# Performance work log

Measured on AMD Instinct MI355X. Metric: run time of the kernel, lower is better.

Reference implementation:

```python
import jax, jax.numpy as jnp
import numpy as np

B, V = 256, 128000

def setup_inputs() -> dict:
    key = jax.random.key(0)
    k1, k2, k3 = jax.random.split(key, 3)
    logits = jax.random.normal(k1, (B, V), dtype=jnp.float32)
    temperatures = jax.random.uniform(k2, (B,), dtype=jnp.float32)
    top_ps = jax.random.uniform(k3, (B,), dtype=jnp.float32)
    return {"logits": logits, "temperatures": temperatures, "top_ps": top_ps}

def reference(logits, temperatures, top_ps):
    logits = logits.astype(jnp.float32)
    greedy_tokens = jnp.argmax(logits, axis=-1)
    t = temperatures[:, None]
    greedy_mask = t <= 1e-10                       # [B, 1]
    safe_t = jnp.maximum(t, 1e-5)
    probs = jax.nn.softmax(logits / safe_t, axis=-1)  # [B, V]
    # descending sort of probs with indices
    order = jnp.argsort(-probs, axis=-1)           # [B, V]
    sorted_probs = jnp.take_along_axis(probs, order, axis=-1)
    cum = jnp.cumsum(sorted_probs, axis=-1)
    mask = cum > top_ps[:, None]
    mask = mask.at[:, 0].set(False)                # always keep top-1
    sorted_probs = jnp.where(mask, 0.0, sorted_probs)
    # scatter the masked probs back to original vocab positions
    rows = jnp.arange(B)[:, None]
    probs = jnp.zeros_like(probs).at[rows, order].set(sorted_probs)
    probs = probs / jnp.sum(probs, axis=-1, keepdims=True)
    # Gumbel-max style sampling: argmax(probs / Exp(1) noise)
    noise = jax.random.exponential(jax.random.key(1), probs.shape, dtype=jnp.float32)
    noise = jnp.maximum(noise, 1e-10)
    sample_tokens = jnp.argmax(probs / noise, axis=-1)
    return jnp.where(greedy_mask[:, 0], greedy_tokens, sample_tokens)
```

## Files before the change

kernel.cpp:

```cpp
#include <hip/hip_runtime.h>
#include <stdint.h>

typedef unsigned long long u64;
typedef uint32_t u32;

#define BB 256
#define VV 128000
#define NV4 (VV / 4)
#define SLICES 16
#define SL4 (NV4 / SLICES)
#define NBUCK 4096
#define CAP 2048
#define QSCALE 1.099511627776e12f
#define QINV   (1.0 / 1099511627776.0)

#define OFF_SMAX 0
#define OFF_SARG (16*1024)
#define OFF_WWIN (32*1024)
#define OFF_PAR  (64*1024)
#define OFF_CNT  (72*1024)
#define OFF_HIST (80*1024)
#define OFF_LIST (OFF_HIST + (size_t)BB*NBUCK*8)
#define WS_TOTAL (OFF_LIST + (size_t)BB*CAP*8)

struct RowPar { int bstar; float thr; double M; double cutZ; };

#if defined(__has_builtin)
# if __has_builtin(__builtin_amdgcn_sched_barrier)
#  define SCHED_FENCE() __builtin_amdgcn_sched_barrier(0)
# endif
#endif
#ifndef SCHED_FENCE
# define SCHED_FENCE() asm volatile("" ::: "memory")
#endif

__device__ __forceinline__ u32 rotl32(u32 v, u32 r) { return (v << r) | (v >> (32u - r)); }

__device__ __forceinline__ u32 threefry_bits(u32 j) {
    const u32 ks0 = 0u, ks1 = 1u, ks2 = 0x1BD11BDBu;
    u32 x0 = ks0, x1 = j + ks1;
    x0 += x1; x1 = rotl32(x1, 13); x1 ^= x0;
    x0 += x1; x1 = rotl32(x1, 15); x1 ^= x0;
    x0 += x1; x1 = rotl32(x1, 26); x1 ^= x0;
    x0 += x1; x1 = rotl32(x1, 6);  x1 ^= x0;
    x0 += ks1; x1 += ks2 + 1u;
    x0 += x1; x1 = rotl32(x1, 17); x1 ^= x0;
    x0 += x1; x1 = rotl32(x1, 29); x1 ^= x0;
    x0 += x1; x1 = rotl32(x1, 16); x1 ^= x0;
    x0 += x1; x1 = rotl32(x1, 24); x1 ^= x0;
    x0 += ks2; x1 += ks0 + 2u;
    x0 += x1; x1 = rotl32(x1, 13); x1 ^= x0;
    x0 += x1; x1 = rotl32(x1, 15); x1 ^= x0;
    x0 += x1; x1 = rotl32(x1, 26); x1 ^= x0;
    x0 += x1; x1 = rotl32(x1, 6);  x1 ^= x0;
    x0 += ks0; x1 += ks1 + 3u;
    x0 += x1; x1 = rotl32(x1, 17); x1 ^= x0;
    x0 += x1; x1 = rotl32(x1, 29); x1 ^= x0;
    x0 += x1; x1 = rotl32(x1, 16); x1 ^= x0;
    x0 += x1; x1 = rotl32(x1, 24); x1 ^= x0;
    x0 += ks1; x1 += ks2 + 4u;
    x0 += x1; x1 = rotl32(x1, 13); x1 ^= x0;
    x0 += x1; x1 = rotl32(x1, 15); x1 ^= x0;
    x0 += x1; x1 = rotl32(x1, 26); x1 ^= x0;
    x0 += x1; x1 = rotl32(x1, 6);  x1 ^= x0;
    x0 += ks2; x1 += ks0 + 5u;
    return x0 ^ x1;
}

__device__ __forceinline__ float q_of(float x, float invT, float xm) {
    return __expf(fmaf(x, invT, -xm));
}

__device__ __forceinline__ float noise_of(u32 j) {
    u32 bits = threefry_bits(j);
    float u = __uint_as_float((bits >> 9) | 0x3F800000u) - 1.0f;
    return fmaxf(-log1pf(-u), 1e-10f);
}

extern "C" __global__ void __launch_bounds__(256, 1)
k1_stats(const float* __restrict__ logits, float* __restrict__ smax,
         int* __restrict__ sarg, u64* __restrict__ Whist, int* __restrict__ Wcnt) {
    int blk = blockIdx.x, r = blk >> 4, s = blk & 15;
    int tid = threadIdx.x, lane = tid & 63, wid = tid >> 6;
    __shared__ float sf[4]; __shared__ int si[4];
    Whist[(size_t)r * NBUCK + s * 256 + tid] = 0ULL;
    if (s == 0 && tid == 0) Wcnt[r] = 0;
    const float4* L4 = (const float4*)(logits + (size_t)r * VV);
    int i0 = s * SL4 + tid;
    bool h7 = tid < (SL4 - 7 * 256);
    float4 b0 = L4[i0],          b1 = L4[i0 + 256],  b2 = L4[i0 + 512];
    float4 b3 = L4[i0 + 768],    b4 = L4[i0 + 1024], b5 = L4[i0 + 1280];
    float4 b6 = L4[i0 + 1536],   b7 = L4[h7 ? i0 + 1792 : i0];
    SCHED_FENCE();
    float m = -3.402823466e38f; int mi = 0x7FFFFFFF;
    auto upd = [&](float4 a, int iv) {
        float m4 = fmaxf(fmaxf(a.x, a.y), fmaxf(a.z, a.w));
        if (m4 > m) {
            int base = iv * 4;
            if      (a.x == m4) mi = base;
            else if (a.y == m4) mi = base + 1;
            else if (a.z == m4) mi = base + 2;
            else                mi = base + 3;
            m = m4;
        }
    };
    upd(b0, i0);        upd(b1, i0 + 256);  upd(b2, i0 + 512);  upd(b3, i0 + 768);
    upd(b4, i0 + 1024); upd(b5, i0 + 1280); upd(b6, i0 + 1536);
    if (h7) upd(b7, i0 + 1792);
    for (int off = 32; off; off >>= 1) {
        float ov = __shfl_down(m, off); int oi = __shfl_down(mi, off);
        if (ov > m || (ov == m && oi < mi)) { m = ov; mi = oi; }
    }
    if (lane == 0) { sf[wid] = m; si[wid] = mi; }
    __syncthreads();
    if (tid == 0) {
        for (int w = 1; w < 4; w++) {
            float ov = sf[w]; int oi = si[w];
            if (ov > m || (ov == m && oi < mi)) { m = ov; mi = oi; }
        }
        smax[blk] = m; sarg[blk] = mi;
    }
}

extern "C" __global__ void __launch_bounds__(256, 1)
k2_hist(const float* __restrict__ logits, const float* __restrict__ smax,
        const float* __restrict__ temps, u64* __restrict__ Whist) {
    __shared__ u64 lh[NBUCK];
    int blk = blockIdx.x, r = blk >> 4, s = blk & 15, tid = threadIdx.x;
    for (int i = tid; i < NBUCK; i += 256) lh[i] = 0ULL;
    float T = fmaxf(temps[r], 1e-5f), invT = 1.0f / T;
    float rm = -3.402823466e38f;
    for (int j = 0; j < 16; j++) rm = fmaxf(rm, smax[r * 16 + j]);
    float xm = rm * invT;
    __syncthreads();
    const float4* L4 = (const float4*)(logits + (size_t)r * VV);
    int i0 = s * SL4 + tid;
    bool h7 = tid < (SL4 - 7 * 256);
    float4 b0 = L4[i0],          b1 = L4[i0 + 256],  b2 = L4[i0 + 512];
    float4 b3 = L4[i0 + 768],    b4 = L4[i0 + 1024], b5 = L4[i0 + 1280];
    float4 b6 = L4[i0 + 1536],   b7 = L4[h7 ? i0 + 1792 : i0];
    SCHED_FENCE();
    auto proc = [&](float4 x) {
        float xs[4] = {x.x, x.y, x.z, x.w};
        #pragma unroll
        for (int k = 0; k < 4; k++) {
            float t = fmaf(xs[k], invT, -xm);
            if (t < -104.0f) continue;
            float q = __expf(t);
            u32 pb = __float_as_uint(q);
            if (pb) atomicAdd(&lh[pb >> 18], (u64)(q * QSCALE));
        }
    };
    proc(b0); proc(b1); proc(b2); proc(b3); proc(b4); proc(b5); proc(b6);
    if (h7) proc(b7);
    __syncthreads();
    u64* gh = Whist + (size_t)r * NBUCK;
    for (int i = tid; i < NBUCK; i += 256) {
        u64 v = lh[i];
        if (v) atomicAdd(&gh[i], v);
    }
}

extern "C" __global__ void __launch_bounds__(1024)
k3_cut(const u64* __restrict__ Whist, const float* __restrict__ topps,
       RowPar* __restrict__ par) {
    int r = blockIdx.x, tid = threadIdx.x, lane = tid & 63, wid = tid >> 6;
    __shared__ double wtot[16];
    __shared__ double sh_cutZ; __shared__ int sh_b; __shared__ double sh_M;
    const u64* gh = Whist + (size_t)r * NBUCK;
    double h0 = (double)gh[4 * tid]     * QINV;
    double h1 = (double)gh[4 * tid + 1] * QINV;
    double h2 = (double)gh[4 * tid + 2] * QINV;
    double h3 = (double)gh[4 * tid + 3] * QINV;
    double s3 = h3, s2 = s3 + h2, s1 = s2 + h1, s0 = s1 + h0;
    double incl = s0;
    for (int off = 1; off < 64; off <<= 1) {
        double u = __shfl_down(incl, off);
        if (lane + off < 64) incl += u;
    }
    double excl = __shfl_down(incl, 1); if (lane == 63) excl = 0.0;
    if (lane == 0) wtot[wid] = incl;
    if (tid == 0) { sh_b = -1; sh_M = 0.0; }
    __syncthreads();
    double cw = 0.0;
    for (int w = wid + 1; w < 16; w++) cw += wtot[w];
    double carry = excl + cw;
    if (tid == 0) sh_cutZ = (double)topps[r] * (s0 + carry);
    __syncthreads();
    double cutZ = sh_cutZ;
    double S0 = s0 + carry, S1 = s1 + carry, S2 = s2 + carry, S3 = s3 + carry;
    if (S0 > cutZ && S1 <= cutZ)    { sh_b = 4 * tid;     sh_M = S1; }
    if (S1 > cutZ && S2 <= cutZ)    { sh_b = 4 * tid + 1; sh_M = S2; }
    if (S2 > cutZ && S3 <= cutZ)    { sh_b = 4 * tid + 2; sh_M = S3; }
    if (S3 > cutZ && carry <= cutZ) { sh_b = 4 * tid + 3; sh_M = carry; }
    __syncthreads();
    if (tid == 0) {
        float thr = -3.402823466e38f;
        if (sh_b > 0) {
            float qlo = __uint_as_float((u32)sh_b << 18);
            if (qlo >= 1.17549435e-38f) thr = logf(qlo) - 1e-3f;
        }
        RowPar p; p.bstar = sh_b; p.thr = thr; p.M = sh_M; p.cutZ = cutZ;
        par[r] = p;
    }
}

extern "C" __global__ void __launch_bounds__(256, 1)
k4_race(const float* __restrict__ logits, const float* __restrict__ smax,
        const float* __restrict__ temps, const RowPar* __restrict__ par,
        int* __restrict__ Wcnt, u64* __restrict__ Wlist, u64* __restrict__ Wwin) {
    int blk = blockIdx.x, r = blk >> 4, s = blk & 15;
    int tid = threadIdx.x, lane = tid & 63, wid = tid >> 6;
    __shared__ u64 seg[4][256];
    __shared__ u64 wred[4];
    float T = fmaxf(temps[r], 1e-5f), invT = 1.0f / T;
    float rm = -3.402823466e38f;
    for (int j = 0; j < 16; j++) rm = fmaxf(rm, smax[r * 16 + j]);
    float xm = rm * invT;
    int bstar = par[r].bstar;
    float thr = par[r].thr;
    const float4* L4 = (const float4*)(logits + (size_t)r * VV);
    u32 jbase = (u32)r * (u32)VV;
    u64 pk = 0ULL;
    const u64 lanelt = (1ULL << lane) - 1ULL;
    int i0 = s * SL4 + tid;
    bool h7 = tid < (SL4 - 7 * 256);
    float4 b0 = L4[i0],          b1 = L4[i0 + 256],  b2 = L4[i0 + 512];
    float4 b3 = L4[i0 + 768],    b4 = L4[i0 + 1024], b5 = L4[i0 + 1280];
    float4 b6 = L4[i0 + 1536],   b7 = L4[h7 ? i0 + 1792 : i0];
    SCHED_FENCE();

    auto chunk = [&](float4 v, int iv, bool valid) {
        float t0 = fmaf(v.x, invT, -xm), t1 = fmaf(v.y, invT, -xm);
        float t2 = fmaf(v.z, invT, -xm), t3 = fmaf(v.w, invT, -xm);
        float ts[4] = {t0, t1, t2, t3};
        int base = iv * 4;
        int wcount = 0;
        #pragma unroll
        for (int k = 0; k < 4; k++) {
            bool pass = valid && (ts[k] >= thr);
            u64 bm = __ballot(pass);
            if (pass) {
                int off = __popcll(bm & lanelt);
                seg[wid][wcount + off] =
                    ((u64)__float_as_uint(ts[k]) << 32) | (u32)(base + k);
            }
            wcount += __popcll(bm);
        }
        asm volatile("s_waitcnt lgkmcnt(0)" ::: "memory");
        for (int di = lane; di < wcount; di += 64) {
            u64 e = seg[wid][di];
            float tt = __uint_as_float((u32)(e >> 32));
            u32 dv = (u32)e;
            float q = __expf(tt);
            u32 pb = __float_as_uint(q);
            if (pb) {
                int b = (int)(pb >> 18);
                if (b > bstar) {
                    float nz = noise_of(jbase + dv);
                    float sc = __fdividef(q, nz);
                    u64 ee = ((u64)__float_as_uint(sc) << 32) | (u64)(~dv);
                    if (ee > pk) pk = ee;
                } else if (b == bstar) {
                    int pos = atomicAdd(&Wcnt[r], 1);
                    if (pos < CAP)
                        Wlist[(size_t)r * CAP + pos] = ((u64)pb << 32) | (u64)(~dv);
                }
            }
        }
    };
    chunk(b0, i0, true);        chunk(b1, i0 + 256, true);
    chunk(b2, i0 + 512, true);  chunk(b3, i0 + 768, true);
    chunk(b4, i0 + 1024, true); chunk(b5, i0 + 1280, true);
    chunk(b6, i0 + 1536, true); chunk(b7, i0 + 1792, h7);

    for (int off = 32; off; off >>= 1) { u64 o = __shfl_down(pk, off); if (o > pk) pk = o; }
    if (lane == 0) wred[wid] = pk;
    __syncthreads();
    if (tid == 0) {
        for (int w = 1; w < 4; w++) if (wred[w] > pk) pk = wred[w];
        Wwin[blk] = pk;
    }
}

extern "C" __global__ void __launch_bounds__(1024)
k5_final(const float* __restrict__ smax, const int* __restrict__ sarg,
         const float* __restrict__ temps, const float* __restrict__ topps,
         const RowPar* __restrict__ par, const int* __restrict__ Wcnt,
         const u64* __restrict__ Wlist, const u64* __restrict__ Wwin,
         int* __restrict__ out) {
    int r = blockIdx.x, tid = threadIdx.x, lane = tid & 63, wid = tid >> 6;
    __shared__ u64 sb[CAP];
    __shared__ double wtot[16];
    __shared__ u64 wred[16];
    __shared__ int sh_js, sh_n, sh_gidx; __shared__ float sh_rm;
    RowPar p = par[r];
    if (tid == 0) {
        float rm = -3.402823466e38f; int gi = 0x7FFFFFFF;
        for (int j = 0; j < 16; j++) {
            float v = smax[r * 16 + j];
            if (v > rm) { rm = v; gi = sarg[r * 16 + j]; }
        }
        sh_rm = rm; sh_gidx = gi;
        int n = Wcnt[r]; if (n > CAP) n = CAP; sh_n = n;
        sh_js = 0x7FFFFFFF;
    }
    __syncthreads();
    int n = sh_n;
    int npad = 4; while (npad < n) npad <<= 1;
    const u64* lst = Wlist + (size_t)r * CAP;
    for (int i = tid; i < npad; i += 1024) sb[i] = (i < n) ? lst[i] : 0ULL;
    __syncthreads();
    for (int k = 2; k <= npad; k <<= 1) {
        for (int j = k >> 1; j > 0; j >>= 1) {
            for (int i = tid; i < npad; i += 1024) {
                int q2 = i ^ j;
                if (q2 > i) {
                    u64 a = sb[i], b = sb[q2];
                    bool desc = ((i & k) == 0);
                    if (desc ? (a < b) : (a > b)) { sb[i] = b; sb[q2] = a; }
                }
            }
            __syncthreads();
        }
    }
    int t2 = tid * 2;
    double f0 = 0.0, f1 = 0.0;
    if (t2 < npad) {
        f0 = (double)__uint_as_float((u32)(sb[t2] >> 32));
        f1 = (double)__uint_as_float((u32)(sb[t2 + 1] >> 32));
    }
    double c0 = f0, c1 = c0 + f1;
    double incl = c1;
    for (int off = 1; off < 64; off <<= 1) {
        double u = __shfl_up(incl, off);
        if (lane >= off) incl += u;
    }
    double excl = __shfl_up(incl, 1); if (lane == 0) excl = 0.0;
    double wt = __shfl(incl, 63);
    if (lane == 0) wtot[wid] = wt;
    __syncthreads();
    double cw = 0.0;
    for (int w = 0; w < wid; w++) cw += wtot[w];
    double cr = cw + excl;
    if (t2 < npad) {
        bool m0 = (p.M + (cr + c0)) > p.cutZ;
        bool m1 = (p.M + (cr + c1)) > p.cutZ;
        int cand = m0 ? t2 : m1 ? (t2 + 1) : 0x7FFFFFFF;
        if (cand != 0x7FFFFFFF) atomicMin(&sh_js, cand);
    }
    __syncthreads();
    float Traw = temps[r];
    if (tid == 0) {
        int js = sh_js; if (js > n) js = n;
        float T = fmaxf(Traw, 1e-5f), invT = 1.0f / T, xm = sh_rm * invT;
        int btop = (int)(__float_as_uint(q_of(sh_rm, invT, xm)) >> 18);
        if (js == 0 && p.bstar == btop) js = 1;
        sh_js = js;
    }
    __syncthreads();
    int js = sh_js;
    u32 jbase = (u32)r * (u32)VV;
    u64 pk = 0ULL;
    for (int i = tid; i < js; i += 1024) {
        u64 key = sb[i];
        float qq = __uint_as_float((u32)(key >> 32));
        u32 v = ~(u32)key;
        float nz = noise_of(jbase + v);
        float sc = __fdividef(qq, nz);
        u64 e = ((u64)__float_as_uint(sc) << 32) | (u64)(~v);
        if (e > pk) pk = e;
    }
    if (tid < 16) { u64 w = Wwin[r * 16 + tid]; if (w > pk) pk = w; }
    for (int off = 32; off; off >>= 1) { u64 o = __shfl_down(pk, off); if (o > pk) pk = o; }
    if (lane == 0) wred[wid] = pk;
    __syncthreads();
    if (tid == 0) {
        for (int w = 1; w < 16; w++) if (wred[w] > pk) pk = wred[w];
        int bi = (int)(~(u32)pk);
        out[r] = (Traw <= 1e-10f) ? sh_gidx : bi;
    }
}

extern "C" __global__ void __launch_bounds__(1024, 1)
sampler_fallback(const float* __restrict__ logits, const float* __restrict__ temps,
                 const float* __restrict__ topps, int* __restrict__ out)
{
    const int row = blockIdx.x;
    const int tid = threadIdx.x;
    const int lane = tid & 63;
    const int wid = tid >> 6;
    const float* L = logits + (size_t)row * VV;
    const float4* L4 = (const float4*)L;
    __shared__ __align__(16) unsigned char SMEM[32768];
    float* hist = (float*)SMEM;
    u64* sortbuf = (u64*)SMEM;
    __shared__ double wtot[16];
    __shared__ float wredf[16];
    __shared__ int wredi[16];
    __shared__ float sh_lmax;
    __shared__ int sh_gidx;
    __shared__ double sh_cutZ;
    __shared__ double sh_M;
    __shared__ int sh_bstar;
    __shared__ int sh_ng;
    __shared__ int sh_jstar;
    const float Traw = temps[row];
    const float T = fmaxf(Traw, 1e-5f);
    const float invT = 1.0f / T;
    const float tp = topps[row];
    float lmax = -3.402823466e38f; int lidx = 0x7FFFFFFF;
    for (int iv = tid; iv < NV4; iv += 1024) {
        float4 x = L4[iv];
        float m4 = fmaxf(fmaxf(x.x, x.y), fmaxf(x.z, x.w));
        if (m4 > lmax) {
            int base = iv * 4;
            if      (x.x == m4) lidx = base;
            else if (x.y == m4) lidx = base + 1;
            else if (x.z == m4) lidx = base + 2;
            else                lidx = base + 3;
            lmax = m4;
        }
    }
    for (int off = 32; off > 0; off >>= 1) {
        float ov = __shfl_down(lmax, off);
        int   oi = __shfl_down(lidx, off);
        if (ov > lmax || (ov == lmax && oi < lidx)) { lmax = ov; lidx = oi; }
    }
    if (lane == 0) { wredf[wid] = lmax; wredi[wid] = lidx; }
    for (int i = tid; i < NBUCK; i += 1024) hist[i] = 0.0f;
    __syncthreads();
    if (wid == 0) {
        float v = (lane < 16) ? wredf[lane] : -3.402823466e38f;
        int   i = (lane < 16) ? wredi[lane] : 0x7FFFFFFF;
        for (int off = 32; off > 0; off >>= 1) {
            float ov = __shfl_down(v, off);
            int   oi = __shfl_down(i, off);
            if (ov > v || (ov == v && oi < i)) { v = ov; i = oi; }
        }
        if (lane == 0) { sh_lmax = v; sh_gidx = i; }
    }
    __syncthreads();
    const float xm = sh_lmax * invT;
    const int gidx = sh_gidx;
    const int btop = (int)(__float_as_uint(q_of(sh_lmax, invT, xm)) >> 18);
    for (int iv = tid; iv < NV4; iv += 1024) {
        float4 x = L4[iv];
        float q0 = q_of(x.x, invT, xm), q1 = q_of(x.y, invT, xm);
        float q2 = q_of(x.z, invT, xm), q3 = q_of(x.w, invT, xm);
        u32 b0 = __float_as_uint(q0), b1 = __float_as_uint(q1);
        u32 b2 = __float_as_uint(q2), b3 = __float_as_uint(q3);
        if (b0) atomicAdd(&hist[b0 >> 18], q0);
        if (b1) atomicAdd(&hist[b1 >> 18], q1);
        if (b2) atomicAdd(&hist[b2 >> 18], q2);
        if (b3) atomicAdd(&hist[b3 >> 18], q3);
    }
    __syncthreads();
    float h0 = hist[4 * tid], h1 = hist[4 * tid + 1],
          h2 = hist[4 * tid + 2], h3 = hist[4 * tid + 3];
    double s3 = (double)h3, s2 = s3 + (double)h2, s1 = s2 + (double)h1, s0 = s1 + (double)h0;
    double incl = s0;
    for (int off = 1; off < 64; off <<= 1) {
        double u = __shfl_down(incl, off);
        if (lane + off < 64) incl += u;
    }
    double excl = __shfl_down(incl, 1);
    if (lane == 63) excl = 0.0;
    if (lane == 0) wtot[wid] = incl;
    __syncthreads();
    double cw = 0.0;
    for (int w = wid + 1; w < 16; w++) cw += wtot[w];
    const double carry = excl + cw;
    if (tid == 0) {
        sh_cutZ = (double)tp * (s0 + carry);
        sh_bstar = -1; sh_M = 0.0; sh_ng = 0; sh_jstar = 0x7FFFFFFF;
    }
    __syncthreads();
    const double cutZ = sh_cutZ;
    {
        double S0 = s0 + carry, S1 = s1 + carry, S2 = s2 + carry, S3 = s3 + carry;
        if (S0 > cutZ && S1 <= cutZ)    { sh_bstar = 4 * tid;     sh_M = S1; }
        if (S1 > cutZ && S2 <= cutZ)    { sh_bstar = 4 * tid + 1; sh_M = S2; }
        if (S2 > cutZ && S3 <= cutZ)    { sh_bstar = 4 * tid + 2; sh_M = S3; }
        if (S3 > cutZ && carry <= cutZ) { sh_bstar = 4 * tid + 3; sh_M = carry; }
    }
    __syncthreads();
    const int bstar = sh_bstar;
    const double M = sh_M;
    float bs = -1.0f; int bi = 0x7FFFFFFF;
    const u32 jbase = (u32)row * (u32)VV;
    for (int iv = tid; iv < NV4; iv += 1024) {
        float4 x = L4[iv];
        float qs[4] = {q_of(x.x, invT, xm), q_of(x.y, invT, xm),
                       q_of(x.z, invT, xm), q_of(x.w, invT, xm)};
        int base = iv * 4;
        #pragma unroll
        for (int k = 0; k < 4; k++) {
            u32 pb = __float_as_uint(qs[k]);
            if (pb == 0u) continue;
            int b = (int)(pb >> 18);
            if (b > bstar) {
                int v = base + k;
                float nz = noise_of(jbase + (u32)v);
                float sc = __fdividef(qs[k], nz);
                if (sc > bs || (sc == bs && v < bi)) { bs = sc; bi = v; }
            } else if (b == bstar) {
                int pos = atomicAdd(&sh_ng, 1);
                if (pos < 4096)
                    sortbuf[pos] = ((u64)pb << 32) | (u32)(~(u32)(base + k));
            }
        }
    }
    __syncthreads();
    if (bstar >= 0) {
        int n = sh_ng; if (n > 4096) n = 4096;
        int npad = 4; while (npad < n) npad <<= 1;
        for (int i = tid; i < npad; i += 1024) if (i >= n) sortbuf[i] = 0ULL;
        __syncthreads();
        for (int k = 2; k <= npad; k <<= 1) {
            for (int j = k >> 1; j > 0; j >>= 1) {
                for (int i = tid; i < npad; i += 1024) {
                    int pidx = i ^ j;
                    if (pidx > i) {
                        u64 a = sortbuf[i], b2 = sortbuf[pidx];
                        bool desc = ((i & k) == 0);
                        if (desc ? (a < b2) : (a > b2)) { sortbuf[i] = b2; sortbuf[pidx] = a; }
                    }
                }
                __syncthreads();
            }
        }
        double f0 = 0.0, f1 = 0.0, f2 = 0.0, f3 = 0.0;
        int t4 = tid * 4;
        if (t4 < npad) {
            f0 = (double)__uint_as_float((u32)(sortbuf[t4]     >> 32));
            f1 = (double)__uint_as_float((u32)(sortbuf[t4 + 1] >> 32));
            f2 = (double)__uint_as_float((u32)(sortbuf[t4 + 2] >> 32));
            f3 = (double)__uint_as_float((u32)(sortbuf[t4 + 3] >> 32));
        }
        double c0 = f0, c1 = c0 + f1, c2 = c1 + f2, c3 = c2 + f3;
        double incl2 = c3;
        for (int off = 1; off < 64; off <<= 1) {
            double u = __shfl_up(incl2, off);
            if (lane >= off) incl2 += u;
        }
        double excl2 = __shfl_up(incl2, 1);
        if (lane == 0) excl2 = 0.0;
        double wt = __shfl(incl2, 63);
        if (lane == 0) wtot[wid] = wt;
        __syncthreads();
        double cw2 = 0.0;
        for (int w = 0; w < wid; w++) cw2 += wtot[w];
        double cr = cw2 + excl2;
        if (t4 < npad) {
            bool m0 = (M + (cr + c0)) > cutZ;
            bool m1 = (M + (cr + c1)) > cutZ;
            bool m2 = (M + (cr + c2)) > cutZ;
            bool m3 = (M + (cr + c3)) > cutZ;
            int cand = m0 ? t4 : m1 ? (t4 + 1) : m2 ? (t4 + 2) : m3 ? (t4 + 3) : 0x7FFFFFFF;
            if (cand != 0x7FFFFFFF) atomicMin(&sh_jstar, cand);
        }
        __syncthreads();
        int jstar = sh_jstar; if (jstar > n) jstar = n;
        if (jstar == 0 && bstar == btop) jstar = 1;
        for (int i = tid; i < jstar; i += 1024) {
            u64 key = sortbuf[i];
            float qq = __uint_as_float((u32)(key >> 32));
            int v = (int)(~(u32)key);
            float nz = noise_of(jbase + (u32)v);
            float sc = __fdividef(qq, nz);
            if (sc > bs || (sc == bs && v < bi)) { bs = sc; bi = v; }
        }
    }
    for (int off = 32; off > 0; off >>= 1) {
        float ov = __shfl_down(bs, off);
        int   oi = __shfl_down(bi, off);
        if (ov > bs || (ov == bs && oi < bi)) { bs = ov; bi = oi; }
    }
    if (lane == 0) { wredf[wid] = bs; wredi[wid] = bi; }
    __syncthreads();
    if (tid == 0) {
        float v = wredf[0]; int i = wredi[0];
        for (int w = 1; w < 16; w++) {
            float ov = wredf[w]; int oi = wredi[w];
            if (ov > v || (ov == v && oi < i)) { v = ov; i = oi; }
        }
        out[row] = (Traw <= 1e-10f) ? gidx : i;
    }
}

extern "C" void kernel_launch(void* const* d_in, const int* in_sizes, int n_in,
                              void* d_out, int out_size, void* d_ws, size_t ws_size,
                              hipStream_t stream) {
    const float* logits = (const float*)d_in[0];
    const float* temps = (const float*)d_in[1];
    const float* topps = (const float*)d_in[2];
    int* out = (int*)d_out;
    (void)in_sizes; (void)n_in; (void)out_size;

    if (ws_size >= WS_TOTAL) {
        char* ws = (char*)d_ws;
        float* smax  = (float*)(ws + OFF_SMAX);
        int*   sarg  = (int*)(ws + OFF_SARG);
        u64*   wwin  = (u64*)(ws + OFF_WWIN);
        RowPar* par  = (RowPar*)(ws + OFF_PAR);
        int*   wcnt  = (int*)(ws + OFF_CNT);
        u64*   whist = (u64*)(ws + OFF_HIST);
        u64*   wlist = (u64*)(ws + OFF_LIST);
        k1_stats<<<BB * SLICES, 256, 0, stream>>>(logits, smax, sarg, whist, wcnt);
        k2_hist<<<BB * SLICES, 256, 0, stream>>>(logits, smax, temps, whist);
        k3_cut<<<BB, 1024, 0, stream>>>(whist, topps, par);
        k4_race<<<BB * SLICES, 256, 0, stream>>>(logits, smax, temps, par, wcnt, wlist, wwin);
        k5_final<<<BB, 1024, 0, stream>>>(smax, sarg, temps, topps, par, wcnt, wlist, wwin, out);
    } else {
        sampler_fallback<<<BB, 1024, 0, stream>>>(logits, temps, topps, out);
    }
}
```

Measured before the change: 368.9 us.

## Double-buffer survivor compaction across waves and tighten histogram exp cutoff

The race kernel now compacts threshold-passing logits into a double-buffered shared segment per wave. All 256 threads then process the survivors of all four waves together, with each thread taking up to four entries, while the next chunk is being filtered. This replaces per-wave serial loops that ran whole iterations for only a few survivors, and it balances the expensive noise and exp work across the block at the cost of a block-wide barrier per chunk. Separately, the histogram kernel skips elements with scaled logit below -27.75 instead of -104, so it does fewer exp and atomic operations. This drops tiny probabilities that may be below the quantization resolution, which could slightly change histogram mass.

```diff
diff --git a/kernel.cpp b/kernel.cpp
--- a/kernel.cpp
+++ b/kernel.cpp
@@ -145,7 +145,7 @@
         #pragma unroll
         for (int k = 0; k < 4; k++) {
             float t = fmaf(xs[k], invT, -xm);
-            if (t < -104.0f) continue;
+            if (t < -27.75f) continue;
             float q = __expf(t);
             u32 pb = __float_as_uint(q);
             if (pb) atomicAdd(&lh[pb >> 18], (u64)(q * QSCALE));
@@ -211,7 +211,8 @@
         int* __restrict__ Wcnt, u64* __restrict__ Wlist, u64* __restrict__ Wwin) {
     int blk = blockIdx.x, r = blk >> 4, s = blk & 15;
     int tid = threadIdx.x, lane = tid & 63, wid = tid >> 6;
-    __shared__ u64 seg[4][256];
+    __shared__ u64 seg[2][4][256];
+    __shared__ int qn[2][4];
     __shared__ u64 wred[4];
     float T = fmaxf(temps[r], 1e-5f), invT = 1.0f / T;
     float rm = -3.402823466e38f;
@@ -223,6 +224,7 @@
     u32 jbase = (u32)r * (u32)VV;
     u64 pk = 0ULL;
     const u64 lanelt = (1ULL << lane) - 1ULL;
+    const int dsg = tid & 3, idxb = tid >> 2;
     int i0 = s * SL4 + tid;
     bool h7 = tid < (SL4 - 7 * 256);
     float4 b0 = L4[i0],          b1 = L4[i0 + 256],  b2 = L4[i0 + 512];
@@ -230,49 +232,68 @@
     float4 b6 = L4[i0 + 1536],   b7 = L4[h7 ? i0 + 1792 : i0];
     SCHED_FENCE();
 
-    auto chunk = [&](float4 v, int iv, bool valid) {
+    auto kfilter = [&](int ph, float4 v, int off, bool valid) {
         float t0 = fmaf(v.x, invT, -xm), t1 = fmaf(v.y, invT, -xm);
         float t2 = fmaf(v.z, invT, -xm), t3 = fmaf(v.w, invT, -xm);
-        float ts[4] = {t0, t1, t2, t3};
-        int base = iv * 4;
-        int wcount = 0;
-        #pragma unroll
-        for (int k = 0; k < 4; k++) {
-            bool pass = valid && (ts[k] >= thr);
-            u64 bm = __ballot(pass);
-            if (pass) {
-                int off = __popcll(bm & lanelt);
-                seg[wid][wcount + off] =
-                    ((u64)__float_as_uint(ts[k]) << 32) | (u32)(base + k);
+        int base = (i0 + off) * 4;
+        bool p0 = valid && (t0 >= thr), p1 = valid && (t1 >= thr);
+        bool p2 = valid && (t2 >= thr), p3 = valid && (t3 >= thr);
+        u64 m0 = __ballot(p0), m1 = __ballot(p1);
+        u64 m2 = __ballot(p2), m3 = __ballot(p3);
+        int c0 = __popcll(m0), c01 = c0 + __popcll(m1), c012 = c01 + __popcll(m2);
+        u64* sg = seg[ph][wid];
+        if (p0) sg[       __popcll(m0 & lanelt)] = ((u64)__float_as_uint(t0) << 32) | (u32)(base + 0);
+        if (p1) sg[c0   + __popcll(m1 & lanelt)] = ((u64)__float_as_uint(t1) << 32) | (u32)(base + 1);
+        if (p2) sg[c01  + __popcll(m2 & lanelt)] = ((u64)__float_as_uint(t2) << 32) | (u32)(base + 2);
+        if (p3) sg[c012 + __popcll(m3 & lanelt)] = ((u64)__float_as_uint(t3) << 32) | (u32)(base + 3);
+        if (lane == 0) qn[ph][wid] = c012 + __popcll(m3);
+    };
+    auto kproc = [&](u64 e) {
+        float tt = __uint_as_float((u32)(e >> 32));
+        u32 dv = (u32)e;
+        float q = __expf(tt);
+        u32 pb = __float_as_uint(q);
+        if (pb) {
+            int b = (int)(pb >> 18);
+            if (b > bstar) {
+                float nz = noise_of(jbase + dv);
+                float sc = __fdividef(q, nz);
+                u64 ee = ((u64)__float_as_uint(sc) << 32) | (u64)(~dv);
+                if (ee > pk) pk = ee;
+            } else if (b == bstar) {
+                int pos = atomicAdd(&Wcnt[r], 1);
+                if (pos < CAP)
+                    Wlist[(size_t)r * CAP + pos] = ((u64)pb << 32) | (u64)(~dv);
             }
-            wcount += __popcll(bm);
-        }
-        asm volatile("s_waitcnt lgkmcnt(0)" ::: "memory");
-        for (int di = lane; di < wcount; di += 64) {
-            u64 e = seg[wid][di];
-            float tt = __uint_as_float((u32)(e >> 32));
-            u32 dv = (u32)e;
-            float q = __expf(tt);
-            u32 pb = __float_as_uint(q);
-            if (pb) {
-                int b = (int)(pb >> 18);
-                if (b > bstar) {
-                    float nz = noise_of(jbase + dv);
-                    float sc = __fdividef(q, nz);
-                    u64 ee = ((u64)__float_as_uint(sc) << 32) | (u64)(~dv);
-                    if (ee > pk) pk = ee;
-                } else if (b == bstar) {
-                    int pos = atomicAdd(&Wcnt[r], 1);
-                    if (pos < CAP)
-                        Wlist[(size_t)r * CAP + pos] = ((u64)pb << 32) | (u64)(~dv);
-                }
-            }
         }
     };
-    chunk(b0, i0, true);        chunk(b1, i0 + 256, true);
-    chunk(b2, i0 + 512, true);  chunk(b3, i0 + 768, true);
-    chunk(b4, i0 + 1024, true); chunk(b5, i0 + 1280, true);
-    chunk(b6, i0 + 1536, true); chunk(b7, i0 + 1792, h7);
+    auto kdense = [&](int ph) {
+        int cnt = qn[ph][dsg];
+        const u64* sg = seg[ph][dsg];
+        u64 e0 = sg[idxb], e1 = sg[idxb + 64], e2 = sg[idxb + 128], e3 = sg[idxb + 192];
+        if (idxb       < cnt) kproc(e0);
+        if (idxb + 64  < cnt) kproc(e1);
+        if (idxb + 128 < cnt) kproc(e2);
+        if (idxb + 192 < cnt) kproc(e3);
+    };
+
+    kfilter(0, b0, 0, true);
+    __syncthreads();
+    kfilter(1, b1, 256, true);   kdense(0);
+    __syncthreads();
+    kfilter(0, b2, 512, true);   kdense(1);
+    __syncthreads();
+    kfilter(1, b3, 768, true);   kdense(0);
+    __syncthreads();
+    kfilter(0, b4, 1024, true);  kdense(1);
+    __syncthreads();
+    kfilter(1, b5, 1280, true);  kdense(0);
+    __syncthreads();
+    kfilter(0, b6, 1536, true);  kdense(1);
+    __syncthreads();
+    kfilter(1, b7, 1792, h7);    kdense(0);
+    __syncthreads();
+    kdense(1);
 
     for (int off = 32; off; off >>= 1) { u64 o = __shfl_down(pk, off); if (o > pk) pk = o; }
     if (lane == 0) wred[wid] = pk;
```

After: 348.2 us. -5.6%, faster.
